# Performance work log

Measured on AMD Instinct MI355X. Metric: run time of the kernel, lower is better.

The kernel has to match this reference:

```python
import jax, jax.numpy as jnp
import numpy as np

B, T = 64, 512
EMBED, HIDDEN, NUM_CLASSES = 512, 1024, 256


def setup_inputs() -> dict:
    key = jax.random.key(0)
    ks = jax.random.split(key, 8)
    x = jax.random.randint(ks[0], (B, T), 0, NUM_CLASSES, dtype=jnp.int32)
    # embedding init uniform(-0.1, 0.1) as in the torch module
    embed = jax.random.uniform(ks[1], (NUM_CLASSES, EMBED), minval=-0.1, maxval=0.1, dtype=jnp.float32)
    s_ih = 1.0 / np.sqrt(HIDDEN)
    W_ih = jax.random.uniform(ks[2], (4 * HIDDEN, EMBED), minval=-s_ih, maxval=s_ih, dtype=jnp.float32)
    W_hh = jax.random.uniform(ks[3], (4 * HIDDEN, HIDDEN), minval=-s_ih, maxval=s_ih, dtype=jnp.float32)
    b_ih = jax.random.uniform(ks[4], (4 * HIDDEN,), minval=-s_ih, maxval=s_ih, dtype=jnp.float32)
    b_hh = jax.random.uniform(ks[5], (4 * HIDDEN,), minval=-s_ih, maxval=s_ih, dtype=jnp.float32)
    s_fc = 1.0 / np.sqrt(HIDDEN)
    fc_W = jax.random.uniform(ks[6], (NUM_CLASSES, HIDDEN), minval=-s_fc, maxval=s_fc, dtype=jnp.float32)
    fc_b = jax.random.uniform(ks[7], (NUM_CLASSES,), minval=-s_fc, maxval=s_fc, dtype=jnp.float32)
    return {"x": x, "embed": embed, "W_ih": W_ih, "W_hh": W_hh,
            "b_ih": b_ih, "b_hh": b_hh, "fc_W": fc_W, "fc_b": fc_b}


def _lstm_forward(x, embed, W_ih, W_hh, b_ih, b_hh, fc_W, fc_b):
    H = W_hh.shape[1]
    x_embed = embed[x]                      # [B, T, E]
    # Precompute input-side gate projections for all timesteps at once.
    gates_x = jnp.einsum('bte,ge->btg', x_embed, W_ih) + (b_ih + b_hh)  # [B, T, 4H]
    gates_x = jnp.transpose(gates_x, (1, 0, 2))  # [T, B, 4H]

    def step(carry, g_x):
        h, c = carry
        gates = g_x + h @ W_hh.T            # [B, 4H]
        i, f, g, o = jnp.split(gates, 4, axis=-1)  # torch gate order: i,f,g,o
        i = jax.nn.sigmoid(i)
        f = jax.nn.sigmoid(f)
        g = jnp.tanh(g)
        o = jax.nn.sigmoid(o)
        c = f * c + i * g
        h = o * jnp.tanh(c)
        return (h, c), h

    Bn = x.shape[0]
    h0 = jnp.zeros((Bn, H), dtype=embed.dtype)
    c0 = jnp.zeros((Bn, H), dtype=embed.dtype)
    _, hs = jax.lax.scan(step, (h0, c0), gates_x)   # hs: [T, B, H]
    hs = jnp.transpose(hs, (1, 0, 2))               # [B, T, H]
    out = jnp.einsum('bth,ch->btc', hs, fc_W) + fc_b  # [B, T, C]
    return out


def reference(x, embed, W_ih, W_hh, b_ih, b_hh, fc_W, fc_b):
    return _lstm_forward(x, embed, W_ih, W_hh, b_ih, b_hh, fc_W, fc_b)
```

## Files before the change

kernel.cpp:

```cpp
#include <hip/hip_runtime.h>
#include <math.h>

#define DEV_INLINE __device__ __forceinline__

static constexpr int Bn = 64;
static constexpr int Tn = 512;
static constexpr int En = 512;
static constexpr int Hn = 1024;
static constexpr int Cn = 256;
static constexpr int Gn = 4 * Hn;

typedef float v4f __attribute__((ext_vector_type(4)));
typedef _Float16 v8h __attribute__((ext_vector_type(8)));

DEV_INLINE float sigmoidf_(float v) { return 1.f / (1.f + __expf(-v)); }

__global__ __launch_bounds__(256) void gemm_tt(
    const float* __restrict__ A, const float* __restrict__ Bm,
    const float* __restrict__ bias1, const float* __restrict__ bias2,
    float* __restrict__ Cm, int M, int N, int K)
{
  constexpr int KC = 32;
  __shared__ float As[KC][68];
  __shared__ float Bs[KC][68];
  const int tid = threadIdx.x;
  const int tx = tid & 15, ty = tid >> 4;
  const int m0 = blockIdx.x * 64, n0 = blockIdx.y * 64;

  float acc[4][4] = {};

  for (int k0 = 0; k0 < K; k0 += KC) {
    __syncthreads();
    #pragma unroll
    for (int j = 0; j < 2; ++j) {
      int f = tid + j * 256;
      int row = f >> 3;
      int c4 = f & 7;
      float4 va = *reinterpret_cast<const float4*>(&A[(size_t)(m0 + row) * K + k0 + c4 * 4]);
      As[c4 * 4 + 0][row] = va.x; As[c4 * 4 + 1][row] = va.y;
      As[c4 * 4 + 2][row] = va.z; As[c4 * 4 + 3][row] = va.w;
      float4 vb = *reinterpret_cast<const float4*>(&Bm[(size_t)(n0 + row) * K + k0 + c4 * 4]);
      Bs[c4 * 4 + 0][row] = vb.x; Bs[c4 * 4 + 1][row] = vb.y;
      Bs[c4 * 4 + 2][row] = vb.z; Bs[c4 * 4 + 3][row] = vb.w;
    }
    __syncthreads();
    #pragma unroll
    for (int k = 0; k < KC; ++k) {
      float4 a4 = *reinterpret_cast<const float4*>(&As[k][ty * 4]);
      float4 b4 = *reinterpret_cast<const float4*>(&Bs[k][tx * 4]);
      float ar[4] = {a4.x, a4.y, a4.z, a4.w};
      float br[4] = {b4.x, b4.y, b4.z, b4.w};
      #pragma unroll
      for (int i = 0; i < 4; ++i)
        #pragma unroll
        for (int j = 0; j < 4; ++j)
          acc[i][j] += ar[i] * br[j];
    }
  }

  #pragma unroll
  for (int j = 0; j < 4; ++j) {
    int n = n0 + tx * 4 + j;
    float bb = bias1[n];
    if (bias2) bb += bias2[n];
    #pragma unroll
    for (int i = 0; i < 4; ++i)
      Cm[(size_t)(m0 + ty * 4 + i) * N + n] = acc[i][j] + bb;
  }
}

__global__ __launch_bounds__(256) void gemm_fc(
    const _Float16* __restrict__ A,
    const float* __restrict__ Bm,
    const float* __restrict__ bias,
    float* __restrict__ out)
{
  constexpr int KC = 32;
  __shared__ float As[KC][68];
  __shared__ float Bs[KC][68];
  const int tid = threadIdx.x;
  const int tx = tid & 15, ty = tid >> 4;
  const int m0 = blockIdx.x * 64, n0 = blockIdx.y * 64;

  float acc[4][4] = {};

  for (int k0 = 0; k0 < Hn; k0 += KC) {
    __syncthreads();
    {
      int row = tid >> 2, c8 = tid & 3;
      v8h va = *(const v8h*)(A + (size_t)(m0 + row) * Hn + k0 + c8 * 8);
      #pragma unroll
      for (int e = 0; e < 8; ++e) As[c8 * 8 + e][row] = (float)va[e];
    }
    #pragma unroll
    for (int j = 0; j < 2; ++j) {
      int f = tid + j * 256, row = f >> 3, c4 = f & 7;
      float4 vb = *reinterpret_cast<const float4*>(&Bm[(size_t)(n0 + row) * Hn + k0 + c4 * 4]);
      Bs[c4 * 4 + 0][row] = vb.x; Bs[c4 * 4 + 1][row] = vb.y;
      Bs[c4 * 4 + 2][row] = vb.z; Bs[c4 * 4 + 3][row] = vb.w;
    }
    __syncthreads();
    #pragma unroll
    for (int k = 0; k < KC; ++k) {
      float4 a4 = *reinterpret_cast<const float4*>(&As[k][ty * 4]);
      float4 b4 = *reinterpret_cast<const float4*>(&Bs[k][tx * 4]);
      float ar[4] = {a4.x, a4.y, a4.z, a4.w};
      float br[4] = {b4.x, b4.y, b4.z, b4.w};
      #pragma unroll
      for (int i = 0; i < 4; ++i)
        #pragma unroll
        for (int j = 0; j < 4; ++j)
          acc[i][j] += ar[i] * br[j];
    }
  }

  #pragma unroll
  for (int j = 0; j < 4; ++j) {
    int n = n0 + tx * 4 + j;
    float bb = bias[n];
    #pragma unroll
    for (int i = 0; i < 4; ++i) {
      int m = m0 + ty * 4 + i;
      int b = m & 63, t = m >> 6;
      out[((size_t)b * Tn + t) * Cn + n] = acc[i][j] + bb;
    }
  }
}

__global__ __launch_bounds__(512, 2) void lstm_mfma(
    const int* __restrict__ x,
    const float* __restrict__ Whh,
    const float* __restrict__ proj,
    _Float16* __restrict__ hs16,
    int* __restrict__ flags)
{
  __shared__ __align__(16) char hT[32768];
  __shared__ float gbuf[128 * 21];
  __shared__ _Float16 hstage[512];

  const int tid = threadIdx.x;
  const int bid = blockIdx.x;
  const int bg = bid >> 5, hg = bid & 31;
  const int b0 = bg * 16;

  const int w = tid >> 6, l = tid & 63;
  const int q = w >> 2, g = w & 3;
  const int mrow = l & 15;
  const int kseg = l >> 4;

  v8h wv[32];
  {
    const float* wr = Whh + (size_t)(g * Hn + hg * 32 + q * 16 + mrow) * Hn + kseg * 8;
    #pragma unroll
    for (int kk = 0; kk < 32; ++kk) {
      const float* p = wr + kk * 32;
      float4 f0 = *(const float4*)p, f1 = *(const float4*)(p + 4);
      v8h h8;
      h8[0] = (_Float16)f0.x; h8[1] = (_Float16)f0.y;
      h8[2] = (_Float16)f0.z; h8[3] = (_Float16)f0.w;
      h8[4] = (_Float16)f1.x; h8[5] = (_Float16)f1.y;
      h8[6] = (_Float16)f1.z; h8[7] = (_Float16)f1.w;
      wv[kk] = h8;
    }
  }

  const int eb = tid >> 5, ehc = tid & 31;
  const int* xp = x + (size_t)(b0 + eb) * Tn;
  float cst = 0.f;

  const int srcoff = (tid & 15) * 2048 + ((tid >> 4) & 3) * 16 + (tid >> 6) * 64;

  for (int t = 0; t < Tn; ++t) {
    const int cls = xp[t];

    if (t > 0) {
      if (tid < 32) {
        const int* fp = flags + ((size_t)(t - 1) * 4 + bg) * 32 + tid;
        int v;
        do {
          asm volatile(
            "global_load_dword %0, %1, off sc0 sc1\n\t"
            "s_waitcnt vmcnt(0)"
            : "=v"(v) : "v"(fp) : "memory");
        } while (v == 0);
      }
      __syncthreads();

      const char* src = (const char*)(hs16 + ((size_t)(t - 1) * Bn + b0) * Hn);
      const char* s0 = src + srcoff;
      v4f r0, r1, r2, r3;
      asm volatile(
        "global_load_dwordx4 %0, %4, off sc0 sc1\n\t"
        "global_load_dwordx4 %1, %5, off sc0 sc1\n\t"
        "global_load_dwordx4 %2, %6, off sc0 sc1\n\t"
        "global_load_dwordx4 %3, %7, off sc0 sc1\n\t"
        "s_waitcnt vmcnt(0)"
        : "=&v"(r0), "=&v"(r1), "=&v"(r2), "=&v"(r3)
        : "v"(s0), "v"(s0 + 512), "v"(s0 + 1024), "v"(s0 + 1536)
        : "memory");
      *(v4f*)(hT + tid * 16 +     0) = r0;
      *(v4f*)(hT + tid * 16 +  8192) = r1;
      *(v4f*)(hT + tid * 16 + 16384) = r2;
      *(v4f*)(hT + tid * 16 + 24576) = r3;
    }
    __syncthreads();

    v4f acc = {0.f, 0.f, 0.f, 0.f};
    if (t > 0) {
      #pragma unroll
      for (int kk = 0; kk < 32; ++kk) {
        v8h a8 = *(const v8h*)(hT + kk * 1024 + l * 16);
        acc = __builtin_amdgcn_mfma_f32_16x16x32_f16(a8, wv[kk], acc, 0, 0, 0);
      }
    }

    #pragma unroll
    for (int r = 0; r < 4; ++r)
      gbuf[(g * 32 + q * 16 + mrow) * 21 + kseg * 4 + r] = acc[r];
    __syncthreads();

    {
      const float* pb = proj + (size_t)cls * Gn + hg * 32 + ehc;
      float g0 = gbuf[(0 * 32 + ehc) * 21 + eb] + pb[0];
      float g1 = gbuf[(1 * 32 + ehc) * 21 + eb] + pb[Hn];
      float g2 = gbuf[(2 * 32 + ehc) * 21 + eb] + pb[2 * Hn];
      float g3 = gbuf[(3 * 32 + ehc) * 21 + eb] + pb[3 * Hn];
      float ig = sigmoidf_(g0), fg = sigmoidf_(g1);
      float gg = tanhf(g2),     og = sigmoidf_(g3);
      cst = fg * cst + ig * gg;
      hstage[eb * 32 + ehc] = (_Float16)(og * tanhf(cst));
    }
    __syncthreads();

    if (tid < 64) {
      const int b = tid >> 2, part = tid & 3;
      v4f v = *(const v4f*)(hstage + b * 32 + part * 8);
      _Float16* dp = hs16 + ((size_t)t * Bn + b0 + b) * Hn + hg * 32 + part * 8;
      asm volatile(
        "global_store_dwordx4 %0, %1, off sc0 sc1\n\t"
        "s_waitcnt vmcnt(0)"
        :: "v"(dp), "v"(v) : "memory");
      if (tid == 0) {
        int one = 1;
        int* fq = flags + ((size_t)t * 4 + bg) * 32 + hg;
        asm volatile(
          "global_store_dword %0, %1, off sc0 sc1\n\t"
          "s_waitcnt vmcnt(0)"
          :: "v"(fq), "v"(one) : "memory");
      }
    }
  }
}

extern "C" void kernel_launch(void* const* d_in, const int* in_sizes, int n_in,
                              void* d_out, int out_size, void* d_ws, size_t ws_size,
                              hipStream_t stream) {
  const int*   x     = (const int*)  d_in[0];
  const float* embed = (const float*)d_in[1];
  const float* Wih   = (const float*)d_in[2];
  const float* Whh   = (const float*)d_in[3];
  const float* bih   = (const float*)d_in[4];
  const float* bhh   = (const float*)d_in[5];
  const float* fcW   = (const float*)d_in[6];
  const float* fcb   = (const float*)d_in[7];
  float* out = (float*)d_out;

  char* ws = (char*)d_ws;
  const size_t ctlBytes  = (size_t)Tn * 4 * 32 * 4;
  const size_t projBytes = (size_t)Cn * Gn * sizeof(float);
  const size_t hsBytes   = (size_t)Tn * Bn * Hn * sizeof(_Float16);
  const size_t need = ctlBytes + projBytes + hsBytes;
  if (ws_size < need) {
    hipMemsetAsync(d_out, 0, (size_t)out_size * sizeof(float), stream);
    return;
  }
  float*     proj = (float*)(ws + ctlBytes);
  _Float16*  hs16 = (_Float16*)(ws + ctlBytes + projBytes);

  hipMemsetAsync(d_ws, 0, ctlBytes, stream);

  dim3 g1(Cn / 64, Gn / 64);
  gemm_tt<<<g1, 256, 0, stream>>>(embed, Wih, bih, bhh, proj, Cn, Gn, En);

  lstm_mfma<<<128, 512, 0, stream>>>(x, Whh, proj, hs16, (int*)d_ws);

  dim3 g3((Bn * Tn) / 64, Cn / 64);
  gemm_fc<<<g3, 256, 0, stream>>>(hs16, fcW, fcb, out);
}
```

Measured before the change: 2.101 ms.

## Replace flag-based inter-block sync with tagged self-validating h exchange buffer

The separate flag array and its spin-wait followed by a second load of h are replaced by a double-buffered exchange buffer. Each 16-byte packet carries four fp16 h values plus a timestep tag, so each thread polls its own data until every tag matches and no separate barrier is needed. The change also drops the store waitcnt, hoists the projection loads ahead of the wait, and splits the MFMA accumulation into two independent chains. This cuts per-step latency on the recurrent critical path but makes the exchange traffic larger, and it depends on each 16-byte store landing atomically.

```diff
diff --git a/kernel.cpp b/kernel.cpp
--- a/kernel.cpp
+++ b/kernel.cpp
@@ -11,6 +11,7 @@
 static constexpr int Gn = 4 * Hn;
 
 typedef float v4f __attribute__((ext_vector_type(4)));
+typedef unsigned int v4u __attribute__((ext_vector_type(4)));
 typedef _Float16 v8h __attribute__((ext_vector_type(8)));
 
 DEV_INLINE float sigmoidf_(float v) { return 1.f / (1.f + __expf(-v)); }
@@ -132,7 +133,7 @@
     const float* __restrict__ Whh,
     const float* __restrict__ proj,
     _Float16* __restrict__ hs16,
-    int* __restrict__ flags)
+    char* __restrict__ xbuf)
 {
   __shared__ __align__(16) char hT[32768];
   __shared__ float gbuf[128 * 21];
@@ -168,63 +169,69 @@
   const int* xp = x + (size_t)(b0 + eb) * Tn;
   float cst = 0.f;
 
-  const int srcoff = (tid & 15) * 2048 + ((tid >> 4) & 3) * 16 + (tid >> 6) * 64;
+  const int csrc = (tid >> 4) * 2048 + (tid & 15) * 128;
+  const int dbase = (tid >> 4) * 1024 + (tid & 15) * 16;
 
   for (int t = 0; t < Tn; ++t) {
     const int cls = xp[t];
+    const float* pb = proj + (size_t)cls * Gn + hg * 32 + ehc;
+    float p0 = pb[0], p1 = pb[Hn], p2 = pb[2 * Hn], p3 = pb[3 * Hn];
 
     if (t > 0) {
-      if (tid < 32) {
-        const int* fp = flags + ((size_t)(t - 1) * 4 + bg) * 32 + tid;
-        int v;
-        do {
-          asm volatile(
-            "global_load_dword %0, %1, off sc0 sc1\n\t"
-            "s_waitcnt vmcnt(0)"
-            : "=v"(v) : "v"(fp) : "memory");
-        } while (v == 0);
+      const unsigned tagv = 0x4000u + (unsigned)(t - 1);
+      const char* pp = xbuf + (size_t)((t - 1) & 1) * 262144 + bg * 65536 + csrc;
+      v4u r0, r1, r2, r3, r4, r5, r6, r7;
+      for (;;) {
+        asm volatile(
+          "global_load_dwordx4 %0, %8, off sc0 sc1\n\t"
+          "global_load_dwordx4 %1, %8, off offset:16 sc0 sc1\n\t"
+          "global_load_dwordx4 %2, %8, off offset:32 sc0 sc1\n\t"
+          "global_load_dwordx4 %3, %8, off offset:48 sc0 sc1\n\t"
+          "global_load_dwordx4 %4, %8, off offset:64 sc0 sc1\n\t"
+          "global_load_dwordx4 %5, %8, off offset:80 sc0 sc1\n\t"
+          "global_load_dwordx4 %6, %8, off offset:96 sc0 sc1\n\t"
+          "global_load_dwordx4 %7, %8, off offset:112 sc0 sc1\n\t"
+          "s_waitcnt vmcnt(0)"
+          : "=&v"(r0), "=&v"(r1), "=&v"(r2), "=&v"(r3),
+            "=&v"(r4), "=&v"(r5), "=&v"(r6), "=&v"(r7)
+          : "v"(pp) : "memory");
+        unsigned m = ((r0.w >> 16) ^ tagv) | ((r1.w >> 16) ^ tagv)
+                   | ((r2.w >> 16) ^ tagv) | ((r3.w >> 16) ^ tagv)
+                   | ((r4.w >> 16) ^ tagv) | ((r5.w >> 16) ^ tagv)
+                   | ((r6.w >> 16) ^ tagv) | ((r7.w >> 16) ^ tagv);
+        if (m == 0u) break;
       }
-      __syncthreads();
-
-      const char* src = (const char*)(hs16 + ((size_t)(t - 1) * Bn + b0) * Hn);
-      const char* s0 = src + srcoff;
-      v4f r0, r1, r2, r3;
-      asm volatile(
-        "global_load_dwordx4 %0, %4, off sc0 sc1\n\t"
-        "global_load_dwordx4 %1, %5, off sc0 sc1\n\t"
-        "global_load_dwordx4 %2, %6, off sc0 sc1\n\t"
-        "global_load_dwordx4 %3, %7, off sc0 sc1\n\t"
-        "s_waitcnt vmcnt(0)"
-        : "=&v"(r0), "=&v"(r1), "=&v"(r2), "=&v"(r3)
-        : "v"(s0), "v"(s0 + 512), "v"(s0 + 1024), "v"(s0 + 1536)
-        : "memory");
-      *(v4f*)(hT + tid * 16 +     0) = r0;
-      *(v4f*)(hT + tid * 16 +  8192) = r1;
-      *(v4f*)(hT + tid * 16 + 16384) = r2;
-      *(v4f*)(hT + tid * 16 + 24576) = r3;
-    }
-    __syncthreads();
-
-    v4f acc = {0.f, 0.f, 0.f, 0.f};
+      v4u rr[8] = {r0, r1, r2, r3, r4, r5, r6, r7};
+      #pragma unroll
+      for (int i = 0; i < 8; ++i) {
+        *(unsigned long long*)(hT + dbase + (i >> 1) * 256 + (i & 1) * 8)
+          = ((unsigned long long)rr[i].y << 32) | (unsigned long long)rr[i].x;
+      }
+    }
+    __syncthreads();
+
+    v4f acc0 = {0.f, 0.f, 0.f, 0.f};
+    v4f acc1 = {0.f, 0.f, 0.f, 0.f};
     if (t > 0) {
       #pragma unroll
-      for (int kk = 0; kk < 32; ++kk) {
-        v8h a8 = *(const v8h*)(hT + kk * 1024 + l * 16);
-        acc = __builtin_amdgcn_mfma_f32_16x16x32_f16(a8, wv[kk], acc, 0, 0, 0);
+      for (int kk = 0; kk < 32; kk += 2) {
+        v8h a0 = *(const v8h*)(hT + kk * 1024 + l * 16);
+        v8h a1 = *(const v8h*)(hT + (kk + 1) * 1024 + l * 16);
+        acc0 = __builtin_amdgcn_mfma_f32_16x16x32_f16(a0, wv[kk], acc0, 0, 0, 0);
+        acc1 = __builtin_amdgcn_mfma_f32_16x16x32_f16(a1, wv[kk + 1], acc1, 0, 0, 0);
       }
     }
 
     #pragma unroll
     for (int r = 0; r < 4; ++r)
-      gbuf[(g * 32 + q * 16 + mrow) * 21 + kseg * 4 + r] = acc[r];
+      gbuf[(g * 32 + q * 16 + mrow) * 21 + kseg * 4 + r] = acc0[r] + acc1[r];
     __syncthreads();
 
     {
-      const float* pb = proj + (size_t)cls * Gn + hg * 32 + ehc;
-      float g0 = gbuf[(0 * 32 + ehc) * 21 + eb] + pb[0];
-      float g1 = gbuf[(1 * 32 + ehc) * 21 + eb] + pb[Hn];
-      float g2 = gbuf[(2 * 32 + ehc) * 21 + eb] + pb[2 * Hn];
-      float g3 = gbuf[(3 * 32 + ehc) * 21 + eb] + pb[3 * Hn];
+      float g0 = gbuf[(0 * 32 + ehc) * 21 + eb] + p0;
+      float g1 = gbuf[(1 * 32 + ehc) * 21 + eb] + p1;
+      float g2 = gbuf[(2 * 32 + ehc) * 21 + eb] + p2;
+      float g3 = gbuf[(3 * 32 + ehc) * 21 + eb] + p3;
       float ig = sigmoidf_(g0), fg = sigmoidf_(g1);
       float gg = tanhf(g2),     og = sigmoidf_(g3);
       cst = fg * cst + ig * gg;
@@ -234,20 +241,22 @@
 
     if (tid < 64) {
       const int b = tid >> 2, part = tid & 3;
-      v4f v = *(const v4f*)(hstage + b * 32 + part * 8);
-      _Float16* dp = hs16 + ((size_t)t * Bn + b0 + b) * Hn + hg * 32 + part * 8;
-      asm volatile(
-        "global_store_dwordx4 %0, %1, off sc0 sc1\n\t"
-        "s_waitcnt vmcnt(0)"
-        :: "v"(dp), "v"(v) : "memory");
-      if (tid == 0) {
-        int one = 1;
-        int* fq = flags + ((size_t)t * 4 + bg) * 32 + hg;
-        asm volatile(
-          "global_store_dword %0, %1, off sc0 sc1\n\t"
-          "s_waitcnt vmcnt(0)"
-          :: "v"(fq), "v"(one) : "memory");
-      }
+      *(v4f*)(hs16 + ((size_t)t * Bn + b0 + b) * Hn + hg * 32 + part * 8)
+        = *(const v4f*)(hstage + b * 32 + part * 8);
+    }
+    if (tid < 128) {
+      const int batch = tid >> 3, cg = tid & 7;
+      unsigned long long d =
+          *(const unsigned long long*)(hstage + batch * 32 + cg * 4);
+      v4u val;
+      val.x = (unsigned)d;
+      val.y = (unsigned)(d >> 32);
+      val.z = 0u;
+      val.w = (0x4000u + (unsigned)t) << 16;
+      char* dst = xbuf + (size_t)(t & 1) * 262144 + bg * 65536
+                + hg * 2048 + tid * 16;
+      asm volatile("global_store_dwordx4 %0, %1, off sc0 sc1"
+                   :: "v"(dst), "v"(val) : "memory");
     }
   }
 }
@@ -266,23 +275,23 @@
   float* out = (float*)d_out;
 
   char* ws = (char*)d_ws;
-  const size_t ctlBytes  = (size_t)Tn * 4 * 32 * 4;
+  const size_t xbufBytes = 524288;
   const size_t projBytes = (size_t)Cn * Gn * sizeof(float);
   const size_t hsBytes   = (size_t)Tn * Bn * Hn * sizeof(_Float16);
-  const size_t need = ctlBytes + projBytes + hsBytes;
+  const size_t need = xbufBytes + projBytes + hsBytes;
   if (ws_size < need) {
     hipMemsetAsync(d_out, 0, (size_t)out_size * sizeof(float), stream);
     return;
   }
-  float*     proj = (float*)(ws + ctlBytes);
-  _Float16*  hs16 = (_Float16*)(ws + ctlBytes + projBytes);
-
-  hipMemsetAsync(d_ws, 0, ctlBytes, stream);
+  float*     proj = (float*)(ws + xbufBytes);
+  _Float16*  hs16 = (_Float16*)(ws + xbufBytes + projBytes);
+
+  hipMemsetAsync(d_ws, 0, xbufBytes, stream);
 
   dim3 g1(Cn / 64, Gn / 64);
   gemm_tt<<<g1, 256, 0, stream>>>(embed, Wih, bih, bhh, proj, Cn, Gn, En);
 
-  lstm_mfma<<<128, 512, 0, stream>>>(x, Whh, proj, hs16, (int*)d_ws);
+  lstm_mfma<<<128, 512, 0, stream>>>(x, Whh, proj, hs16, ws);
 
   dim3 g3((Bn * Tn) / 64, Cn / 64);
   gemm_fc<<<g3, 256, 0, stream>>>(hs16, fcW, fcb, out);
```

Result: slower. 2.774 ms (+32.0%).

## Interleave two batch groups per LSTM block and halve the recurrent grid

Applied to the files above, without the earlier changes.

Each block now processes two 16-row batch groups in alternation, sharing one copy of the fp16 W_hh slice held in registers, so the grid drops from 128 to 64 blocks. The idea is that while one group waits on its cross-block flag, the other group's step can make progress, hiding synchronisation latency. The MFMA chain is split into two independent accumulators to shorten the dependency chain, and the input-projection loads are hoisted ahead of the flag wait. The trade-off is that each block now does twice the serial work per timestep with half as many blocks in flight.

```diff
diff --git a/kernel.cpp b/kernel.cpp
--- a/kernel.cpp
+++ b/kernel.cpp
@@ -140,8 +140,7 @@
 
   const int tid = threadIdx.x;
   const int bid = blockIdx.x;
-  const int bg = bid >> 5, hg = bid & 31;
-  const int b0 = bg * 16;
+  const int pair = bid >> 5, hg = bid & 31;
 
   const int w = tid >> 6, l = tid & 63;
   const int q = w >> 2, g = w & 3;
@@ -165,88 +164,98 @@
   }
 
   const int eb = tid >> 5, ehc = tid & 31;
-  const int* xp = x + (size_t)(b0 + eb) * Tn;
-  float cst = 0.f;
+  const int* xp0 = x + (size_t)((pair * 2 + 0) * 16 + eb) * Tn;
+  const int* xp1 = x + (size_t)((pair * 2 + 1) * 16 + eb) * Tn;
+  float cst[2] = {0.f, 0.f};
 
   const int srcoff = (tid & 15) * 2048 + ((tid >> 4) & 3) * 16 + (tid >> 6) * 64;
 
   for (int t = 0; t < Tn; ++t) {
-    const int cls = xp[t];
-
-    if (t > 0) {
-      if (tid < 32) {
-        const int* fp = flags + ((size_t)(t - 1) * 4 + bg) * 32 + tid;
-        int v;
-        do {
+    #pragma unroll
+    for (int s = 0; s < 2; ++s) {
+      const int bg = pair * 2 + s;
+      const int b0 = bg * 16;
+      const int cls = (s == 0) ? xp0[t] : xp1[t];
+      const float* pb = proj + (size_t)cls * Gn + hg * 32 + ehc;
+      float p0 = pb[0], p1 = pb[Hn], p2 = pb[2 * Hn], p3 = pb[3 * Hn];
+
+      if (t > 0) {
+        if (tid < 32) {
+          const int* fp = flags + ((size_t)(t - 1) * 4 + bg) * 32 + tid;
+          int v;
+          do {
+            asm volatile(
+              "global_load_dword %0, %1, off sc0 sc1\n\t"
+              "s_waitcnt vmcnt(0)"
+              : "=v"(v) : "v"(fp) : "memory");
+          } while (v == 0);
+        }
+        __syncthreads();
+
+        const char* src = (const char*)(hs16 + ((size_t)(t - 1) * Bn + b0) * Hn);
+        const char* s0 = src + srcoff;
+        v4f r0, r1, r2, r3;
+        asm volatile(
+          "global_load_dwordx4 %0, %4, off sc0 sc1\n\t"
+          "global_load_dwordx4 %1, %5, off sc0 sc1\n\t"
+          "global_load_dwordx4 %2, %6, off sc0 sc1\n\t"
+          "global_load_dwordx4 %3, %7, off sc0 sc1\n\t"
+          "s_waitcnt vmcnt(0)"
+          : "=&v"(r0), "=&v"(r1), "=&v"(r2), "=&v"(r3)
+          : "v"(s0), "v"(s0 + 512), "v"(s0 + 1024), "v"(s0 + 1536)
+          : "memory");
+        *(v4f*)(hT + tid * 16 +     0) = r0;
+        *(v4f*)(hT + tid * 16 +  8192) = r1;
+        *(v4f*)(hT + tid * 16 + 16384) = r2;
+        *(v4f*)(hT + tid * 16 + 24576) = r3;
+      }
+      __syncthreads();
+
+      v4f acc0 = {0.f, 0.f, 0.f, 0.f};
+      v4f acc1 = {0.f, 0.f, 0.f, 0.f};
+      if (t > 0) {
+        #pragma unroll
+        for (int kk = 0; kk < 32; kk += 2) {
+          v8h a0 = *(const v8h*)(hT + kk * 1024 + l * 16);
+          v8h a1 = *(const v8h*)(hT + (kk + 1) * 1024 + l * 16);
+          acc0 = __builtin_amdgcn_mfma_f32_16x16x32_f16(a0, wv[kk], acc0, 0, 0, 0);
+          acc1 = __builtin_amdgcn_mfma_f32_16x16x32_f16(a1, wv[kk + 1], acc1, 0, 0, 0);
+        }
+      }
+
+      #pragma unroll
+      for (int r = 0; r < 4; ++r)
+        gbuf[(g * 32 + q * 16 + mrow) * 21 + kseg * 4 + r] = acc0[r] + acc1[r];
+      __syncthreads();
+
+      {
+        float g0 = gbuf[(0 * 32 + ehc) * 21 + eb] + p0;
+        float g1 = gbuf[(1 * 32 + ehc) * 21 + eb] + p1;
+        float g2 = gbuf[(2 * 32 + ehc) * 21 + eb] + p2;
+        float g3 = gbuf[(3 * 32 + ehc) * 21 + eb] + p3;
+        float ig = sigmoidf_(g0), fg = sigmoidf_(g1);
+        float gg = tanhf(g2),     og = sigmoidf_(g3);
+        cst[s] = fg * cst[s] + ig * gg;
+        hstage[eb * 32 + ehc] = (_Float16)(og * tanhf(cst[s]));
+      }
+      __syncthreads();
+
+      if (tid < 64) {
+        const int b = tid >> 2, part = tid & 3;
+        v4f v = *(const v4f*)(hstage + b * 32 + part * 8);
+        _Float16* dp = hs16 + ((size_t)t * Bn + b0 + b) * Hn + hg * 32 + part * 8;
+        asm volatile(
+          "global_store_dwordx4 %0, %1, off sc0 sc1\n\t"
+          "s_waitcnt vmcnt(0)"
+          :: "v"(dp), "v"(v) : "memory");
+        if (tid == 0) {
+          int one = 1;
+          int* fq = flags + ((size_t)t * 4 + bg) * 32 + hg;
           asm volatile(
-            "global_load_dword %0, %1, off sc0 sc1\n\t"
+            "global_store_dword %0, %1, off sc0 sc1\n\t"
             "s_waitcnt vmcnt(0)"
-            : "=v"(v) : "v"(fp) : "memory");
-        } while (v == 0);
-      }
-      __syncthreads();
-
-      const char* src = (const char*)(hs16 + ((size_t)(t - 1) * Bn + b0) * Hn);
-      const char* s0 = src + srcoff;
-      v4f r0, r1, r2, r3;
-      asm volatile(
-        "global_load_dwordx4 %0, %4, off sc0 sc1\n\t"
-        "global_load_dwordx4 %1, %5, off sc0 sc1\n\t"
-        "global_load_dwordx4 %2, %6, off sc0 sc1\n\t"
-        "global_load_dwordx4 %3, %7, off sc0 sc1\n\t"
-        "s_waitcnt vmcnt(0)"
-        : "=&v"(r0), "=&v"(r1), "=&v"(r2), "=&v"(r3)
-        : "v"(s0), "v"(s0 + 512), "v"(s0 + 1024), "v"(s0 + 1536)
-        : "memory");
-      *(v4f*)(hT + tid * 16 +     0) = r0;
-      *(v4f*)(hT + tid * 16 +  8192) = r1;
-      *(v4f*)(hT + tid * 16 + 16384) = r2;
-      *(v4f*)(hT + tid * 16 + 24576) = r3;
-    }
-    __syncthreads();
-
-    v4f acc = {0.f, 0.f, 0.f, 0.f};
-    if (t > 0) {
-      #pragma unroll
-      for (int kk = 0; kk < 32; ++kk) {
-        v8h a8 = *(const v8h*)(hT + kk * 1024 + l * 16);
-        acc = __builtin_amdgcn_mfma_f32_16x16x32_f16(a8, wv[kk], acc, 0, 0, 0);
-      }
-    }
-
-    #pragma unroll
-    for (int r = 0; r < 4; ++r)
-      gbuf[(g * 32 + q * 16 + mrow) * 21 + kseg * 4 + r] = acc[r];
-    __syncthreads();
-
-    {
-      const float* pb = proj + (size_t)cls * Gn + hg * 32 + ehc;
-      float g0 = gbuf[(0 * 32 + ehc) * 21 + eb] + pb[0];
-      float g1 = gbuf[(1 * 32 + ehc) * 21 + eb] + pb[Hn];
-      float g2 = gbuf[(2 * 32 + ehc) * 21 + eb] + pb[2 * Hn];
-      float g3 = gbuf[(3 * 32 + ehc) * 21 + eb] + pb[3 * Hn];
-      float ig = sigmoidf_(g0), fg = sigmoidf_(g1);
-      float gg = tanhf(g2),     og = sigmoidf_(g3);
-      cst = fg * cst + ig * gg;
-      hstage[eb * 32 + ehc] = (_Float16)(og * tanhf(cst));
-    }
-    __syncthreads();
-
-    if (tid < 64) {
-      const int b = tid >> 2, part = tid & 3;
-      v4f v = *(const v4f*)(hstage + b * 32 + part * 8);
-      _Float16* dp = hs16 + ((size_t)t * Bn + b0 + b) * Hn + hg * 32 + part * 8;
-      asm volatile(
-        "global_store_dwordx4 %0, %1, off sc0 sc1\n\t"
-        "s_waitcnt vmcnt(0)"
-        :: "v"(dp), "v"(v) : "memory");
-      if (tid == 0) {
-        int one = 1;
-        int* fq = flags + ((size_t)t * 4 + bg) * 32 + hg;
-        asm volatile(
-          "global_store_dword %0, %1, off sc0 sc1\n\t"
-          "s_waitcnt vmcnt(0)"
-          :: "v"(fq), "v"(one) : "memory");
+            :: "v"(fq), "v"(one) : "memory");
+        }
       }
     }
   }
@@ -282,7 +291,7 @@
   dim3 g1(Cn / 64, Gn / 64);
   gemm_tt<<<g1, 256, 0, stream>>>(embed, Wih, bih, bhh, proj, Cn, Gn, En);
 
-  lstm_mfma<<<128, 512, 0, stream>>>(x, Whh, proj, hs16, (int*)d_ws);
+  lstm_mfma<<<64, 512, 0, stream>>>(x, Whh, proj, hs16, (int*)d_ws);
 
   dim3 g3((Bn * Tn) / 64, Cn / 64);
   gemm_fc<<<g3, 256, 0, stream>>>(hs16, fcW, fcb, out);
```

After: 3.588 ms. 1.71x slower.

## Fuse FC projection into LSTM kernel with consumer blocks and remap gate layout

Applied to the files above, without the earlier changes.

Launches 256 blocks in place of 128. The first 128 blocks run the recurrence and the extra 128 poll per-timestep flags and compute the FC output with fp16 MFMA as soon as each h_t is ready, so the separate fp32 FC GEMM overlaps the serial scan. The recurrent weight rows are reordered so each lane's MFMA output holds all four gates for one (batch, hidden) element, which removes the gbuf LDS round-trip and one barrier per step. The MFMA chain is also split into two accumulators, and fcW is converted to fp16 in a small pre-kernel. The approach depends on all 256 blocks being co-resident to avoid deadlock, and the consumer blocks add memory traffic that could interfere with the latency-critical recurrence.

```diff
diff --git a/kernel.cpp b/kernel.cpp
--- a/kernel.cpp
+++ b/kernel.cpp
@@ -69,184 +69,205 @@
   }
 }
 
-__global__ __launch_bounds__(256) void gemm_fc(
-    const _Float16* __restrict__ A,
-    const float* __restrict__ Bm,
-    const float* __restrict__ bias,
-    float* __restrict__ out)
+__global__ __launch_bounds__(256) void cvt_fcw(
+    const float* __restrict__ fcW, _Float16* __restrict__ fcW16)
 {
-  constexpr int KC = 32;
-  __shared__ float As[KC][68];
-  __shared__ float Bs[KC][68];
-  const int tid = threadIdx.x;
-  const int tx = tid & 15, ty = tid >> 4;
-  const int m0 = blockIdx.x * 64, n0 = blockIdx.y * 64;
-
-  float acc[4][4] = {};
-
-  for (int k0 = 0; k0 < Hn; k0 += KC) {
-    __syncthreads();
-    {
-      int row = tid >> 2, c8 = tid & 3;
-      v8h va = *(const v8h*)(A + (size_t)(m0 + row) * Hn + k0 + c8 * 8);
-      #pragma unroll
-      for (int e = 0; e < 8; ++e) As[c8 * 8 + e][row] = (float)va[e];
-    }
-    #pragma unroll
-    for (int j = 0; j < 2; ++j) {
-      int f = tid + j * 256, row = f >> 3, c4 = f & 7;
-      float4 vb = *reinterpret_cast<const float4*>(&Bm[(size_t)(n0 + row) * Hn + k0 + c4 * 4]);
-      Bs[c4 * 4 + 0][row] = vb.x; Bs[c4 * 4 + 1][row] = vb.y;
-      Bs[c4 * 4 + 2][row] = vb.z; Bs[c4 * 4 + 3][row] = vb.w;
-    }
-    __syncthreads();
-    #pragma unroll
-    for (int k = 0; k < KC; ++k) {
-      float4 a4 = *reinterpret_cast<const float4*>(&As[k][ty * 4]);
-      float4 b4 = *reinterpret_cast<const float4*>(&Bs[k][tx * 4]);
-      float ar[4] = {a4.x, a4.y, a4.z, a4.w};
-      float br[4] = {b4.x, b4.y, b4.z, b4.w};
-      #pragma unroll
-      for (int i = 0; i < 4; ++i)
-        #pragma unroll
-        for (int j = 0; j < 4; ++j)
-          acc[i][j] += ar[i] * br[j];
-    }
-  }
-
-  #pragma unroll
-  for (int j = 0; j < 4; ++j) {
-    int n = n0 + tx * 4 + j;
-    float bb = bias[n];
-    #pragma unroll
-    for (int i = 0; i < 4; ++i) {
-      int m = m0 + ty * 4 + i;
-      int b = m & 63, t = m >> 6;
-      out[((size_t)b * Tn + t) * Cn + n] = acc[i][j] + bb;
-    }
-  }
+  const int idx = (blockIdx.x * 256 + threadIdx.x) * 8;
+  float4 f0 = *(const float4*)(fcW + idx);
+  float4 f1 = *(const float4*)(fcW + idx + 4);
+  v8h h8;
+  h8[0] = (_Float16)f0.x; h8[1] = (_Float16)f0.y;
+  h8[2] = (_Float16)f0.z; h8[3] = (_Float16)f0.w;
+  h8[4] = (_Float16)f1.x; h8[5] = (_Float16)f1.y;
+  h8[6] = (_Float16)f1.z; h8[7] = (_Float16)f1.w;
+  *(v8h*)(fcW16 + idx) = h8;
 }
 
-__global__ __launch_bounds__(512, 2) void lstm_mfma(
+__global__ __launch_bounds__(512, 2) void lstm_fused(
     const int* __restrict__ x,
     const float* __restrict__ Whh,
     const float* __restrict__ proj,
     _Float16* __restrict__ hs16,
-    int* __restrict__ flags)
+    int* __restrict__ flags,
+    const _Float16* __restrict__ fcW16,
+    const float* __restrict__ fcb,
+    float* __restrict__ out)
 {
   __shared__ __align__(16) char hT[32768];
-  __shared__ float gbuf[128 * 21];
   __shared__ _Float16 hstage[512];
 
   const int tid = threadIdx.x;
   const int bid = blockIdx.x;
-  const int bg = bid >> 5, hg = bid & 31;
-  const int b0 = bg * 16;
 
   const int w = tid >> 6, l = tid & 63;
-  const int q = w >> 2, g = w & 3;
   const int mrow = l & 15;
   const int kseg = l >> 4;
 
-  v8h wv[32];
-  {
-    const float* wr = Whh + (size_t)(g * Hn + hg * 32 + q * 16 + mrow) * Hn + kseg * 8;
-    #pragma unroll
-    for (int kk = 0; kk < 32; ++kk) {
-      const float* p = wr + kk * 32;
-      float4 f0 = *(const float4*)p, f1 = *(const float4*)(p + 4);
-      v8h h8;
-      h8[0] = (_Float16)f0.x; h8[1] = (_Float16)f0.y;
-      h8[2] = (_Float16)f0.z; h8[3] = (_Float16)f0.w;
-      h8[4] = (_Float16)f1.x; h8[5] = (_Float16)f1.y;
-      h8[6] = (_Float16)f1.z; h8[7] = (_Float16)f1.w;
-      wv[kk] = h8;
-    }
-  }
-
-  const int eb = tid >> 5, ehc = tid & 31;
-  const int* xp = x + (size_t)(b0 + eb) * Tn;
-  float cst = 0.f;
-
   const int srcoff = (tid & 15) * 2048 + ((tid >> 4) & 3) * 16 + (tid >> 6) * 64;
 
-  for (int t = 0; t < Tn; ++t) {
-    const int cls = xp[t];
-
-    if (t > 0) {
+  if (bid < 128) {
+    const int bg = bid >> 5, hg = bid & 31;
+    const int b0 = bg * 16;
+
+    v8h wv[32];
+    {
+      const float* wr = Whh
+        + (size_t)((mrow & 3) * Hn + hg * 32 + w * 4 + (mrow >> 2)) * Hn
+        + kseg * 8;
+      #pragma unroll
+      for (int kk = 0; kk < 32; ++kk) {
+        const float* p = wr + kk * 32;
+        float4 f0 = *(const float4*)p, f1 = *(const float4*)(p + 4);
+        v8h h8;
+        h8[0] = (_Float16)f0.x; h8[1] = (_Float16)f0.y;
+        h8[2] = (_Float16)f0.z; h8[3] = (_Float16)f0.w;
+        h8[4] = (_Float16)f1.x; h8[5] = (_Float16)f1.y;
+        h8[6] = (_Float16)f1.z; h8[7] = (_Float16)f1.w;
+        wv[kk] = h8;
+      }
+    }
+
+    const int eb = mrow;
+    const int ehc = w * 4 + kseg;
+    const int* xp = x + (size_t)(b0 + eb) * Tn;
+    float cst = 0.f;
+
+    for (int t = 0; t < Tn; ++t) {
+      const int cls = xp[t];
+      const float* pb = proj + (size_t)cls * Gn + hg * 32 + ehc;
+      float p0 = pb[0], p1 = pb[Hn], p2 = pb[2 * Hn], p3 = pb[3 * Hn];
+
+      if (t > 0) {
+        if (tid < 32) {
+          const int* fp = flags + ((size_t)(t - 1) * 4 + bg) * 32 + tid;
+          int v;
+          do {
+            asm volatile(
+              "global_load_dword %0, %1, off sc0 sc1\n\t"
+              "s_waitcnt vmcnt(0)"
+              : "=v"(v) : "v"(fp) : "memory");
+          } while (v == 0);
+        }
+        __syncthreads();
+
+        const char* src = (const char*)(hs16 + ((size_t)(t - 1) * Bn + b0) * Hn);
+        const char* s0 = src + srcoff;
+        v4f r0, r1, r2, r3;
+        asm volatile(
+          "global_load_dwordx4 %0, %4, off sc0 sc1\n\t"
+          "global_load_dwordx4 %1, %5, off sc0 sc1\n\t"
+          "global_load_dwordx4 %2, %6, off sc0 sc1\n\t"
+          "global_load_dwordx4 %3, %7, off sc0 sc1\n\t"
+          "s_waitcnt vmcnt(0)"
+          : "=&v"(r0), "=&v"(r1), "=&v"(r2), "=&v"(r3)
+          : "v"(s0), "v"(s0 + 512), "v"(s0 + 1024), "v"(s0 + 1536)
+          : "memory");
+        *(v4f*)(hT + tid * 16 +     0) = r0;
+        *(v4f*)(hT + tid * 16 +  8192) = r1;
+        *(v4f*)(hT + tid * 16 + 16384) = r2;
+        *(v4f*)(hT + tid * 16 + 24576) = r3;
+      }
+      __syncthreads();
+
+      v4f acc0 = {0.f, 0.f, 0.f, 0.f};
+      v4f acc1 = {0.f, 0.f, 0.f, 0.f};
+      if (t > 0) {
+        #pragma unroll
+        for (int kk = 0; kk < 32; kk += 2) {
+          v8h a0 = *(const v8h*)(hT + kk * 1024 + l * 16);
+          v8h a1 = *(const v8h*)(hT + (kk + 1) * 1024 + l * 16);
+          acc0 = __builtin_amdgcn_mfma_f32_16x16x32_f16(wv[kk], a0, acc0, 0, 0, 0);
+          acc1 = __builtin_amdgcn_mfma_f32_16x16x32_f16(wv[kk + 1], a1, acc1, 0, 0, 0);
+        }
+      }
+
+      {
+        float g0 = acc0[0] + acc1[0] + p0;
+        float g1 = acc0[1] + acc1[1] + p1;
+        float g2 = acc0[2] + acc1[2] + p2;
+        float g3 = acc0[3] + acc1[3] + p3;
+        float ig = sigmoidf_(g0), fg = sigmoidf_(g1);
+        float gg = tanhf(g2),     og = sigmoidf_(g3);
+        cst = fg * cst + ig * gg;
+        hstage[eb * 32 + ehc] = (_Float16)(og * tanhf(cst));
+      }
+      __syncthreads();
+
+      if (tid < 64) {
+        const int b = tid >> 2, part = tid & 3;
+        v4f v = *(const v4f*)(hstage + b * 32 + part * 8);
+        _Float16* dp = hs16 + ((size_t)t * Bn + b0 + b) * Hn + hg * 32 + part * 8;
+        asm volatile(
+          "global_store_dwordx4 %0, %1, off sc0 sc1\n\t"
+          "s_waitcnt vmcnt(0)"
+          :: "v"(dp), "v"(v) : "memory");
+        if (tid == 0) {
+          int one = 1;
+          int* fq = flags + ((size_t)t * 4 + bg) * 32 + hg;
+          asm volatile(
+            "global_store_dword %0, %1, off sc0 sc1\n\t"
+            "s_waitcnt vmcnt(0)"
+            :: "v"(fq), "v"(one) : "memory");
+        }
+      }
+    }
+  } else {
+    const int fid = bid - 128;
+
+    for (int j = 0; j < 16; ++j) {
+      const int unit = j * 128 + fid;
+      const int t = unit >> 2, bgf = unit & 3;
+      const int b0f = bgf * 16;
+
       if (tid < 32) {
-        const int* fp = flags + ((size_t)(t - 1) * 4 + bg) * 32 + tid;
+        const int* fp = flags + ((size_t)t * 4 + bgf) * 32 + tid;
         int v;
-        do {
+        for (;;) {
           asm volatile(
             "global_load_dword %0, %1, off sc0 sc1\n\t"
             "s_waitcnt vmcnt(0)"
             : "=v"(v) : "v"(fp) : "memory");
-        } while (v == 0);
+          if (v != 0) break;
+          __builtin_amdgcn_s_sleep(16);
+        }
       }
       __syncthreads();
 
-      const char* src = (const char*)(hs16 + ((size_t)(t - 1) * Bn + b0) * Hn);
-      const char* s0 = src + srcoff;
-      v4f r0, r1, r2, r3;
-      asm volatile(
-        "global_load_dwordx4 %0, %4, off sc0 sc1\n\t"
-        "global_load_dwordx4 %1, %5, off sc0 sc1\n\t"
-        "global_load_dwordx4 %2, %6, off sc0 sc1\n\t"
-        "global_load_dwordx4 %3, %7, off sc0 sc1\n\t"
-        "s_waitcnt vmcnt(0)"
-        : "=&v"(r0), "=&v"(r1), "=&v"(r2), "=&v"(r3)
-        : "v"(s0), "v"(s0 + 512), "v"(s0 + 1024), "v"(s0 + 1536)
-        : "memory");
-      *(v4f*)(hT + tid * 16 +     0) = r0;
-      *(v4f*)(hT + tid * 16 +  8192) = r1;
-      *(v4f*)(hT + tid * 16 + 16384) = r2;
-      *(v4f*)(hT + tid * 16 + 24576) = r3;
-    }
-    __syncthreads();
-
-    v4f acc = {0.f, 0.f, 0.f, 0.f};
-    if (t > 0) {
+      {
+        const char* src = (const char*)(hs16 + ((size_t)t * Bn + b0f) * Hn);
+        const char* s0 = src + srcoff;
+        v4f r0, r1, r2, r3;
+        asm volatile(
+          "global_load_dwordx4 %0, %4, off sc0 sc1\n\t"
+          "global_load_dwordx4 %1, %5, off sc0 sc1\n\t"
+          "global_load_dwordx4 %2, %6, off sc0 sc1\n\t"
+          "global_load_dwordx4 %3, %7, off sc0 sc1\n\t"
+          "s_waitcnt vmcnt(0)"
+          : "=&v"(r0), "=&v"(r1), "=&v"(r2), "=&v"(r3)
+          : "v"(s0), "v"(s0 + 512), "v"(s0 + 1024), "v"(s0 + 1536)
+          : "memory");
+        *(v4f*)(hT + tid * 16 +     0) = r0;
+        *(v4f*)(hT + tid * 16 +  8192) = r1;
+        *(v4f*)(hT + tid * 16 + 16384) = r2;
+        *(v4f*)(hT + tid * 16 + 24576) = r3;
+      }
+      __syncthreads();
+
       #pragma unroll
-      for (int kk = 0; kk < 32; ++kk) {
-        v8h a8 = *(const v8h*)(hT + kk * 1024 + l * 16);
-        acc = __builtin_amdgcn_mfma_f32_16x16x32_f16(a8, wv[kk], acc, 0, 0, 0);
-      }
-    }
-
-    #pragma unroll
-    for (int r = 0; r < 4; ++r)
-      gbuf[(g * 32 + q * 16 + mrow) * 21 + kseg * 4 + r] = acc[r];
-    __syncthreads();
-
-    {
-      const float* pb = proj + (size_t)cls * Gn + hg * 32 + ehc;
-      float g0 = gbuf[(0 * 32 + ehc) * 21 + eb] + pb[0];
-      float g1 = gbuf[(1 * 32 + ehc) * 21 + eb] + pb[Hn];
-      float g2 = gbuf[(2 * 32 + ehc) * 21 + eb] + pb[2 * Hn];
-      float g3 = gbuf[(3 * 32 + ehc) * 21 + eb] + pb[3 * Hn];
-      float ig = sigmoidf_(g0), fg = sigmoidf_(g1);
-      float gg = tanhf(g2),     og = sigmoidf_(g3);
-      cst = fg * cst + ig * gg;
-      hstage[eb * 32 + ehc] = (_Float16)(og * tanhf(cst));
-    }
-    __syncthreads();
-
-    if (tid < 64) {
-      const int b = tid >> 2, part = tid & 3;
-      v4f v = *(const v4f*)(hstage + b * 32 + part * 8);
-      _Float16* dp = hs16 + ((size_t)t * Bn + b0 + b) * Hn + hg * 32 + part * 8;
-      asm volatile(
-        "global_store_dwordx4 %0, %1, off sc0 sc1\n\t"
-        "s_waitcnt vmcnt(0)"
-        :: "v"(dp), "v"(v) : "memory");
-      if (tid == 0) {
-        int one = 1;
-        int* fq = flags + ((size_t)t * 4 + bg) * 32 + hg;
-        asm volatile(
-          "global_store_dword %0, %1, off sc0 sc1\n\t"
-          "s_waitcnt vmcnt(0)"
-          :: "v"(fq), "v"(one) : "memory");
+      for (int nt = 0; nt < 2; ++nt) {
+        const int clsbase = w * 32 + nt * 16;
+        v4f acc = {0.f, 0.f, 0.f, 0.f};
+        const _Float16* ab = fcW16 + (size_t)(clsbase + mrow) * Hn + kseg * 8;
+        #pragma unroll
+        for (int kk = 0; kk < 32; ++kk) {
+          v8h af = *(const v8h*)(ab + kk * 32);
+          v8h bf = *(const v8h*)(hT + kk * 1024 + l * 16);
+          acc = __builtin_amdgcn_mfma_f32_16x16x32_f16(af, bf, acc, 0, 0, 0);
+        }
+        v4f b4 = *(const v4f*)(fcb + clsbase + kseg * 4);
+        v4f res = {acc[0] + b4[0], acc[1] + b4[1], acc[2] + b4[2], acc[3] + b4[3]};
+        float* op = out + ((size_t)(b0f + mrow) * Tn + t) * Cn + clsbase + kseg * 4;
+        *(v4f*)op = res;
       }
     }
   }
@@ -266,24 +287,26 @@
   float* out = (float*)d_out;
 
   char* ws = (char*)d_ws;
-  const size_t ctlBytes  = (size_t)Tn * 4 * 32 * 4;
+  const size_t flagBytes = (size_t)Tn * 4 * 32 * 4;
   const size_t projBytes = (size_t)Cn * Gn * sizeof(float);
   const size_t hsBytes   = (size_t)Tn * Bn * Hn * sizeof(_Float16);
-  const size_t need = ctlBytes + projBytes + hsBytes;
+  const size_t fw16Bytes = (size_t)Cn * Hn * sizeof(_Float16);
+  const size_t need = flagBytes + projBytes + hsBytes + fw16Bytes;
   if (ws_size < need) {
     hipMemsetAsync(d_out, 0, (size_t)out_size * sizeof(float), stream);
     return;
   }
-  float*     proj = (float*)(ws + ctlBytes);
-  _Float16*  hs16 = (_Float16*)(ws + ctlBytes + projBytes);
-
-  hipMemsetAsync(d_ws, 0, ctlBytes, stream);
+  float*     proj  = (float*)(ws + flagBytes);
+  _Float16*  hs16  = (_Float16*)(ws + flagBytes + projBytes);
+  _Float16*  fcW16 = (_Float16*)(ws + flagBytes + projBytes + hsBytes);
+
+  hipMemsetAsync(d_ws, 0, flagBytes, stream);
+
+  cvt_fcw<<<128, 256, 0, stream>>>(fcW, fcW16);
 
   dim3 g1(Cn / 64, Gn / 64);
   gemm_tt<<<g1, 256, 0, stream>>>(embed, Wih, bih, bhh, proj, Cn, Gn, En);
 
-  lstm_mfma<<<128, 512, 0, stream>>>(x, Whh, proj, hs16, (int*)d_ws);
-
-  dim3 g3((Bn * Tn) / 64, Cn / 64);
-  gemm_fc<<<g3, 256, 0, stream>>>(hs16, fcW, fcb, out);
+  lstm_fused<<<256, 512, 0, stream>>>(x, Whh, proj, hs16, (int*)d_ws,
+                                      fcW16, fcb, out);
 }
```

Result: faster. 1.992 ms (-5.2%).
